# Performance work log

Hardware: AMD Instinct MI355X
Metric: run time of the kernel (lower is better)

Reference implementation:

```python
import jax, jax.numpy as jnp
import numpy as np

C = 4          # number of classes (cloud-organization dataset has 4)
EMPTY = 1.0    # IoU value when a class is absent from both pred and label


def setup_inputs() -> dict:
    key = jax.random.key(0)
    k1, k2 = jax.random.split(key)
    shape = (16, 1024, 1024)
    # preds are hard class predictions (stored as float, integer-valued)
    preds = jax.random.randint(k1, shape, 0, C).astype(jnp.float32)
    labels = jax.random.randint(k2, shape, 0, C).astype(jnp.int32)
    return {"preds": preds, "labels": labels}


def reference(preds, labels):
    # Vectorized form of the per-class loop:
    #   intersection_i = ((label == i) & (pred == i)).sum()
    #   union_i        = ((label == i) | (pred == i)).sum()   (ignore=None)
    cls = jnp.arange(C)                      # [C]
    pm = preds[..., None] == cls             # [B,H,W,C] bool
    lm = labels[..., None] == cls            # [B,H,W,C] bool
    inter = jnp.sum(pm & lm, axis=(0, 1, 2)).astype(jnp.float32)  # [C]
    union = jnp.sum(pm | lm, axis=(0, 1, 2)).astype(jnp.float32)  # [C]
    ious = jnp.where(union == 0, EMPTY, inter / jnp.where(union == 0, 1.0, union))
    ious_pct = 100.0 * ious                  # matches 100 * np.array(ious)
    return 1.0 - ious_pct                    # forward returns 1 - iou, shape [C]
```

## Files before the change

kernel.cpp:

```cpp
#include <hip/hip_runtime.h>


#define NCLS 4

__global__ __launch_bounds__(256) void iou_count_kernel(
    const float4* __restrict__ preds,
    const int4*   __restrict__ labels,
    unsigned int* __restrict__ counters,
    int n4)
{
    int cnt_i[NCLS] = {0, 0, 0, 0};
    int cnt_p[NCLS] = {0, 0, 0, 0};
    int cnt_l[NCLS] = {0, 0, 0, 0};

    const int tid    = blockIdx.x * blockDim.x + threadIdx.x;
    const int stride = gridDim.x * blockDim.x;

    for (int idx = tid; idx < n4; idx += stride) {
        const float4 p = preds[idx];
        const int4   l = labels[idx];
        const int ip0 = (int)p.x, ip1 = (int)p.y, ip2 = (int)p.z, ip3 = (int)p.w;

#pragma unroll
        for (int c = 0; c < NCLS; ++c) {
            const int pm0 = (ip0 == c), lm0 = (l.x == c);
            const int pm1 = (ip1 == c), lm1 = (l.y == c);
            const int pm2 = (ip2 == c), lm2 = (l.z == c);
            const int pm3 = (ip3 == c), lm3 = (l.w == c);
            cnt_i[c] += (pm0 & lm0) + (pm1 & lm1) + (pm2 & lm2) + (pm3 & lm3);
            cnt_p[c] += pm0 + pm1 + pm2 + pm3;
            cnt_l[c] += lm0 + lm1 + lm2 + lm3;
        }
    }

#pragma unroll
    for (int c = 0; c < NCLS; ++c) {
#pragma unroll
        for (int off = 32; off > 0; off >>= 1) {
            cnt_i[c] += __shfl_down(cnt_i[c], off);
            cnt_p[c] += __shfl_down(cnt_p[c], off);
            cnt_l[c] += __shfl_down(cnt_l[c], off);
        }
    }

    __shared__ unsigned int s[3 * NCLS];
    if (threadIdx.x < 3 * NCLS) s[threadIdx.x] = 0u;
    __syncthreads();

    if ((threadIdx.x & 63) == 0) {
#pragma unroll
        for (int c = 0; c < NCLS; ++c) {
            atomicAdd(&s[c],            (unsigned int)cnt_i[c]);
            atomicAdd(&s[NCLS + c],     (unsigned int)cnt_p[c]);
            atomicAdd(&s[2 * NCLS + c], (unsigned int)cnt_l[c]);
        }
    }
    __syncthreads();

    if (threadIdx.x < 3 * NCLS)
        atomicAdd(&counters[threadIdx.x], s[threadIdx.x]);
}

__global__ void iou_finalize_kernel(const unsigned int* __restrict__ counters,
                                    float* __restrict__ out)
{
    const int c = threadIdx.x;
    if (c < NCLS) {
        const float inter = (float)counters[c];
        const float uni   = (float)(counters[NCLS + c] + counters[2 * NCLS + c]
                                    - counters[c]);
        const float iou   = (uni == 0.0f) ? 1.0f : (inter / uni);
        out[c] = 1.0f - 100.0f * iou;
    }
}

extern "C" void kernel_launch(void* const* d_in, const int* in_sizes, int n_in,
                              void* d_out, int out_size, void* d_ws, size_t ws_size,
                              hipStream_t stream) {
    const float4* preds  = (const float4*)d_in[0];
    const int4*   labels = (const int4*)d_in[1];
    unsigned int* counters = (unsigned int*)d_ws;
    float* out = (float*)d_out;

    const int n  = in_sizes[0];
    const int n4 = n / 4;

    hipMemsetAsync(counters, 0, 3 * NCLS * sizeof(unsigned int), stream);

    const int threads = 256;
    const int blocks  = 1024;
    iou_count_kernel<<<blocks, threads, 0, stream>>>(preds, labels, counters, n4);
    iou_finalize_kernel<<<1, 64, 0, stream>>>(counters, out);
}
```

Before: 150.6 us.

## Fuse finalize into count kernel via last-block pattern, unroll loads, double grid

Merges the separate finalize kernel into the counting kernel using an atomic block counter, so the last block to finish computes the IoU outputs. The main loop is unrolled four-way, issuing eight vector loads per iteration to raise memory-level parallelism. The grid grows from 1024 to 2048 blocks. The aim is to remove one kernel launch and better saturate HBM bandwidth, at the cost of an extra atomic and fence per block.

```diff
diff --git a/kernel.cpp b/kernel.cpp
--- a/kernel.cpp
+++ b/kernel.cpp
@@ -3,10 +3,11 @@
 
 #define NCLS 4
 
-__global__ __launch_bounds__(256) void iou_count_kernel(
+__global__ __launch_bounds__(256) void iou_fused_kernel(
     const float4* __restrict__ preds,
     const int4*   __restrict__ labels,
-    unsigned int* __restrict__ counters,
+    unsigned int* __restrict__ ws,
+    float* __restrict__ out,
     int n4)
 {
     int cnt_i[NCLS] = {0, 0, 0, 0};
@@ -16,11 +17,8 @@
     const int tid    = blockIdx.x * blockDim.x + threadIdx.x;
     const int stride = gridDim.x * blockDim.x;
 
-    for (int idx = tid; idx < n4; idx += stride) {
-        const float4 p = preds[idx];
-        const int4   l = labels[idx];
+    auto acc = [&](const float4 p, const int4 l) {
         const int ip0 = (int)p.x, ip1 = (int)p.y, ip2 = (int)p.z, ip3 = (int)p.w;
-
 #pragma unroll
         for (int c = 0; c < NCLS; ++c) {
             const int pm0 = (ip0 == c), lm0 = (l.x == c);
@@ -31,7 +29,22 @@
             cnt_p[c] += pm0 + pm1 + pm2 + pm3;
             cnt_l[c] += lm0 + lm1 + lm2 + lm3;
         }
+    };
+
+    int idx = tid;
+    for (; idx + 3 * stride < n4; idx += 4 * stride) {
+        const float4 p0 = preds[idx];
+        const float4 p1 = preds[idx + stride];
+        const float4 p2 = preds[idx + 2 * stride];
+        const float4 p3 = preds[idx + 3 * stride];
+        const int4   l0 = labels[idx];
+        const int4   l1 = labels[idx + stride];
+        const int4   l2 = labels[idx + 2 * stride];
+        const int4   l3 = labels[idx + 3 * stride];
+        acc(p0, l0); acc(p1, l1); acc(p2, l2); acc(p3, l3);
     }
+    for (; idx < n4; idx += stride)
+        acc(preds[idx], labels[idx]);
 
 #pragma unroll
     for (int c = 0; c < NCLS; ++c) {
@@ -44,6 +57,7 @@
     }
 
     __shared__ unsigned int s[3 * NCLS];
+    __shared__ int is_last;
     if (threadIdx.x < 3 * NCLS) s[threadIdx.x] = 0u;
     __syncthreads();
 
@@ -58,17 +72,21 @@
     __syncthreads();
 
     if (threadIdx.x < 3 * NCLS)
-        atomicAdd(&counters[threadIdx.x], s[threadIdx.x]);
-}
+        atomicAdd(&ws[threadIdx.x], s[threadIdx.x]);
 
-__global__ void iou_finalize_kernel(const unsigned int* __restrict__ counters,
-                                    float* __restrict__ out)
-{
-    const int c = threadIdx.x;
-    if (c < NCLS) {
-        const float inter = (float)counters[c];
-        const float uni   = (float)(counters[NCLS + c] + counters[2 * NCLS + c]
-                                    - counters[c]);
+    __threadfence();
+    if (threadIdx.x == 0) {
+        const unsigned t = atomicAdd(&ws[12], 1u);
+        is_last = (t == gridDim.x - 1);
+    }
+    __syncthreads();
+
+    if (is_last && threadIdx.x < NCLS) {
+        const int c = threadIdx.x;
+        const float inter = (float)atomicAdd(&ws[c], 0u);
+        const float cp    = (float)atomicAdd(&ws[NCLS + c], 0u);
+        const float cl    = (float)atomicAdd(&ws[2 * NCLS + c], 0u);
+        const float uni   = cp + cl - inter;
         const float iou   = (uni == 0.0f) ? 1.0f : (inter / uni);
         out[c] = 1.0f - 100.0f * iou;
     }
@@ -79,16 +97,15 @@
                               hipStream_t stream) {
     const float4* preds  = (const float4*)d_in[0];
     const int4*   labels = (const int4*)d_in[1];
-    unsigned int* counters = (unsigned int*)d_ws;
+    unsigned int* ws  = (unsigned int*)d_ws;
     float* out = (float*)d_out;
 
     const int n  = in_sizes[0];
     const int n4 = n / 4;
 
-    hipMemsetAsync(counters, 0, 3 * NCLS * sizeof(unsigned int), stream);
+    hipMemsetAsync(ws, 0, 13 * sizeof(unsigned int), stream);
 
     const int threads = 256;
-    const int blocks  = 1024;
-    iou_count_kernel<<<blocks, threads, 0, stream>>>(preds, labels, counters, n4);
-    iou_finalize_kernel<<<1, 64, 0, stream>>>(counters, out);
+    const int blocks  = 2048;
+    iou_fused_kernel<<<blocks, threads, 0, stream>>>(preds, labels, ws, out, n4);
 }
```

Result: slower. 318.1 us (+111.3%).
